# Optimization experiments

Measured on AMD Instinct MI355X. Metric: run time of the kernel, lower is better.

## Reference

```python
import jax, jax.numpy as jnp
import numpy as np

N = 50000      # nodes per graph
E = 800000     # edges per graph (avg degree 16)
IN = 128       # in_dim
OUT = 64       # out_dim
HEADS = 2      # second GCNConv out = OUT*HEADS = 128
FILL = 2.0     # improved=True self-loop weight


def setup_inputs():
    key = jax.random.key(0)
    ks = jax.random.split(key, 10)
    x1 = jax.random.normal(ks[0], (N, IN), jnp.float32)
    edge_index1 = jax.random.randint(ks[1], (2, E), 0, N)
    edge_weight1 = jax.random.uniform(ks[2], (E,), jnp.float32)
    x2 = jax.random.normal(ks[3], (N, IN), jnp.float32)
    edge_index2 = jax.random.randint(ks[4], (2, E), 0, N)
    edge_weight2 = jax.random.uniform(ks[5], (E,), jnp.float32)
    # shared tower params (source bug: gcn1 used for both inputs)
    W1 = jax.random.normal(ks[6], (IN, OUT), jnp.float32) / np.sqrt(IN)
    b1 = jnp.zeros((OUT,), jnp.float32)
    W2 = jax.random.normal(ks[7], (OUT, OUT * HEADS), jnp.float32) / np.sqrt(OUT)
    b2 = jnp.zeros((OUT * HEADS,), jnp.float32)
    return {"x1": x1, "edge_index1": edge_index1, "edge_weight1": edge_weight1,
            "x2": x2, "edge_index2": edge_index2, "edge_weight2": edge_weight2,
            "W1": W1, "b1": b1, "W2": W2, "b2": b2}


def _gcn_conv(x, src, dst, ew, W, b, n):
    # GCNConv(improved=True, add_self_loops=True, aggr='max')
    loop = jnp.arange(n)
    src = jnp.concatenate([src, loop])
    dst = jnp.concatenate([dst, loop])
    ew = jnp.concatenate([ew, jnp.full((n,), FILL, ew.dtype)])
    # symmetric gcn normalization
    deg = jax.ops.segment_sum(ew, dst, num_segments=n)
    dinv = jnp.where(deg > 0, jax.lax.rsqrt(jnp.maximum(deg, 1e-30)), 0.0)
    norm = dinv[src] * ew * dinv[dst]          # [E+N]
    h = x @ W                                   # [N, F_out]
    msg = norm[:, None] * h[src]                # [E+N, F_out] gathered messages
    out = jax.ops.segment_max(msg, dst, num_segments=n)  # scatter-max
    out = jnp.where(jnp.isfinite(out), out, 0.0)          # guard empty segments
    return out + b


def _tower(x, ei, ew, W1, b1, W2, b2):
    ew = jax.nn.relu(ew)
    h = _gcn_conv(x, ei[0], ei[1], ew, W1, b1, x.shape[0])
    return _gcn_conv(h, ei[0], ei[1], ew, W2, b2, x.shape[0])


def reference(x1, edge_index1, edge_weight1, x2, edge_index2, edge_weight2, W1, b1, W2, b2):
    g1 = _tower(x1, edge_index1, edge_weight1, W1, b1, W2, b2)
    g2 = _tower(x2, edge_index2, edge_weight2, W1, b1, W2, b2)
    return (g1, g2)
```

## Files before the change

### kernel.cpp

```cpp
#include <hip/hip_runtime.h>
#include <hip/hip_fp16.h>

static constexpr float FILLW = 2.0f;
static constexpr int BSH  = 6;
static constexpr int CAPB = 1792;
static constexpr int NPB  = 256;
static constexpr int EPT  = 8;

__device__ __forceinline__ unsigned pk_mul(unsigned a, unsigned b){
    unsigned r; asm("v_pk_mul_f16 %0, %1, %2" : "=v"(r) : "v"(a), "v"(b)); return r;
}
__device__ __forceinline__ unsigned pk_max(unsigned a, unsigned b){
    unsigned r; asm("v_pk_max_f16 %0, %1, %2" : "=v"(r) : "v"(a), "v"(b)); return r;
}

template<int F, int K, int TR, int KC, bool SCALE, typename OutT>
__device__ __forceinline__ void gemm_tile(const float* __restrict__ A,
        const float* __restrict__ W, OutT* __restrict__ C,
        const float* __restrict__ dv, int rb, int N,
        float* __restrict__ Ws, float* __restrict__ As){
    constexpr int NCH = K / KC;
    constexpr int TRp = TR + 4;
    constexpr int CG  = F / 8;
    constexpr int LPT = TR * KC / 1024;
    const int tid = threadIdx.x;
    for (int i = tid; i < K * F / 4; i += 256)
        ((float4*)Ws)[i] = ((const float4*)W)[i];
    const int tx = tid % CG, ty = tid / CG;
    const int c0 = tx * 8, r0 = ty * 8;

    float acc[8][8];
    #pragma unroll
    for (int i = 0; i < 8; ++i)
        #pragma unroll
        for (int j = 0; j < 8; ++j) acc[i][j] = 0.f;

    float4 st[LPT];
    auto gload = [&](int kc){
        #pragma unroll
        for (int l2 = 0; l2 < LPT; ++l2){
            int l = l2 * 256 + tid;
            int r = l / (KC / 4);
            int kk = (l % (KC / 4)) * 4;
            int ar = rb + r; if (ar >= N) ar = N - 1;
            st[l2] = *(const float4*)(A + (size_t)ar * K + kc * KC + kk);
        }
    };
    auto swrite = [&](int buf){
        float* p = As + buf * (KC * TRp);
        #pragma unroll
        for (int l2 = 0; l2 < LPT; ++l2){
            int l = l2 * 256 + tid;
            int r = l / (KC / 4);
            int kk = (l % (KC / 4)) * 4;
            p[(kk+0)*TRp + r] = st[l2].x;
            p[(kk+1)*TRp + r] = st[l2].y;
            p[(kk+2)*TRp + r] = st[l2].z;
            p[(kk+3)*TRp + r] = st[l2].w;
        }
    };

    gload(0); swrite(0);
    __syncthreads();
    for (int kc = 0; kc < NCH; ++kc){
        if (kc + 1 < NCH) gload(kc + 1);
        const float* Ab = As + (kc & 1) * (KC * TRp);
        #pragma unroll
        for (int j = 0; j < KC; ++j){
            const float* wrow = Ws + (kc * KC + j) * F + c0;
            float4 w0 = *(const float4*)(wrow);
            float4 w1 = *(const float4*)(wrow + 4);
            float4 a0 = *(const float4*)(Ab + j * TRp + r0);
            float4 a1 = *(const float4*)(Ab + j * TRp + r0 + 4);
            float av[8] = {a0.x,a0.y,a0.z,a0.w,a1.x,a1.y,a1.z,a1.w};
            float wvv[8] = {w0.x,w0.y,w0.z,w0.w,w1.x,w1.y,w1.z,w1.w};
            #pragma unroll
            for (int rr = 0; rr < 8; ++rr)
                #pragma unroll
                for (int cc = 0; cc < 8; ++cc)
                    acc[rr][cc] = fmaf(av[rr], wvv[cc], acc[rr][cc]);
        }
        if (kc + 1 < NCH){ swrite((kc + 1) & 1); __syncthreads(); }
    }
    #pragma unroll
    for (int rr = 0; rr < 8; ++rr){
        int row = rb + r0 + rr;
        if (row < N){
            float scv = 1.0f;
            if constexpr (SCALE) scv = dv[row];
            if constexpr (sizeof(OutT) == 2){
                __half2 o2[4];
                #pragma unroll
                for (int q = 0; q < 4; ++q)
                    o2[q] = __floats2half2_rn(acc[rr][2*q]*scv, acc[rr][2*q+1]*scv);
                *(float4*)((__half*)C + (size_t)row * F + c0) = *(float4*)o2;
            } else {
                float4 o0 = {acc[rr][0]*scv, acc[rr][1]*scv, acc[rr][2]*scv, acc[rr][3]*scv};
                float4 o1 = {acc[rr][4]*scv, acc[rr][5]*scv, acc[rr][6]*scv, acc[rr][7]*scv};
                *(float4*)((float*)C + (size_t)row * F + c0)     = o0;
                *(float4*)((float*)C + (size_t)row * F + c0 + 4) = o1;
            }
        }
    }
}

__device__ __forceinline__ void xcd_map(int c, int TW2, int LIN_BPT,
                                        int& t, int& chunk){
    if (TW2){ int x = c & 7; t = x >> 2; chunk = (c >> 3) * 4 + (x & 3); }
    else    { t = c / LIN_BPT; chunk = c - t * LIN_BPT; }
}

__global__ void __launch_bounds__(256) k_cg1(const float* __restrict__ x0,
        const float* __restrict__ x1, const float* __restrict__ W1,
        __half* __restrict__ h0, __half* __restrict__ h1,
        const int* __restrict__ dst0, const int* __restrict__ dst1,
        int* __restrict__ cnts,
        int N, int E, int BPT, int GB, int B1, int TW2){
    __shared__ float Ws[64 * 128];
    __shared__ float As[2 * 8 * 260];
    if ((int)blockIdx.x < GB){
        int t  = (int)blockIdx.x / BPT;
        int rb = ((int)blockIdx.x - t * BPT) * 256;
        gemm_tile<64,128,256,8,false,__half>(t ? x1 : x0, W1, t ? h1 : h0,
                                             nullptr, rb, N, Ws, As);
        return;
    }
    int t, blk;
    xcd_map((int)blockIdx.x - GB, TW2, NPB, t, blk);
    const int* dst = t ? dst1 : dst0;
    int* hist = (int*)Ws;
    const int tid = threadIdx.x;
    for (int i = tid; i < B1; i += 256) hist[i] = 0;
    __syncthreads();
    int per = (E + NPB - 1) / NPB;
    int e0 = blk * per;
    int e1 = e0 + per; if (e1 > E) e1 = E;
    for (int e = e0 + tid; e < e1; e += 256 * EPT){
        int dl[EPT];
        #pragma unroll
        for (int q = 0; q < EPT; ++q){ int ee = e + q*256; dl[q] = (ee < e1) ? dst[ee] : -1; }
        #pragma unroll
        for (int q = 0; q < EPT; ++q) if (dl[q] >= 0) atomicAdd(&hist[dl[q] >> BSH], 1);
    }
    __syncthreads();
    int* co = cnts + (size_t)(t * NPB + blk) * B1;
    for (int i = tid; i < B1; i += 256) co[i] = hist[i];
}

__global__ void __launch_bounds__(64) k_scanR(int* __restrict__ cnts,
        int* __restrict__ gcnt, int B1){
    int bid = (int)blockIdx.x;
    int t = bid / B1, b = bid % B1;
    int lane = threadIdx.x;
    int* cp = cnts + (size_t)t * NPB * B1 + b;
    int x[4];
    #pragma unroll
    for (int j = 0; j < 4; ++j) x[j] = cp[(size_t)(lane * 4 + j) * B1];
    int s = x[0] + x[1] + x[2] + x[3];
    int sc = s;
    #pragma unroll
    for (int o = 1; o < 64; o <<= 1){ int u = __shfl_up(sc, o); if (lane >= o) sc += u; }
    int e0 = sc - s;
    int e1 = e0 + x[0], e2 = e1 + x[1], e3 = e2 + x[2];
    cp[(size_t)(lane * 4 + 0) * B1] = e0;
    cp[(size_t)(lane * 4 + 1) * B1] = e1;
    cp[(size_t)(lane * 4 + 2) * B1] = e2;
    cp[(size_t)(lane * 4 + 3) * B1] = e3;
    if (lane == 63) gcnt[t * B1 + b] = sc;
}

__global__ void __launch_bounds__(256) k_scatter(const int* __restrict__ src0,
        const int* __restrict__ src1,
        const int* __restrict__ dst0, const int* __restrict__ dst1,
        const float* __restrict__ ew0, const float* __restrict__ ew1,
        const int* __restrict__ cnts, uint2* __restrict__ stage,
        int N, int E, int B1, int TW2){
    __shared__ int hist[1024];
    int t, blk;
    xcd_map((int)blockIdx.x, TW2, NPB, t, blk);
    const int* src = t ? src1 : src0;
    const int* dst = t ? dst1 : dst0;
    const float* ew = t ? ew1 : ew0;
    uint2* stg = stage + (size_t)t * B1 * CAPB;
    const int* co = cnts + (size_t)(t * NPB + blk) * B1;
    const int tid = threadIdx.x;
    for (int i = tid; i < B1; i += 256) hist[i] = co[i];
    __syncthreads();
    int per = (E + NPB - 1) / NPB;
    int e0 = blk * per;
    int e1 = e0 + per; if (e1 > E) e1 = E;
    for (int e = e0 + tid; e < e1; e += 256 * EPT){
        int dl[EPT], sl[EPT]; float wl[EPT];
        #pragma unroll
        for (int q = 0; q < EPT; ++q){
            int ee = e + q*256;
            if (ee < e1){ dl[q] = dst[ee]; sl[q] = src[ee]; wl[q] = fmaxf(ew[ee], 0.f); }
            else dl[q] = -1;
        }
        int r[EPT];
        #pragma unroll
        for (int q = 0; q < EPT; ++q)
            if (dl[q] >= 0) r[q] = atomicAdd(&hist[dl[q] >> BSH], 1);
        #pragma unroll
        for (int q = 0; q < EPT; ++q)
            if (dl[q] >= 0 && r[q] < CAPB)
                stg[(size_t)(dl[q] >> BSH) * CAPB + r[q]] =
                    make_uint2(__float_as_uint(wl[q]),
                               (unsigned)sl[q] | ((unsigned)(dl[q] & 63) << 16));
    }
}

__global__ void __launch_bounds__(256) k_pack(const uint2* __restrict__ stage,
        const int* __restrict__ gcnt, int* __restrict__ woff,
        uint2* __restrict__ sn, float* __restrict__ dinv,
        __half* __restrict__ h1, int N, int E, int B1, int TW2){
    int t, b;
    xcd_map((int)blockIdx.x, TW2, B1, t, b);
    if (b >= B1) return;
    const int tid = threadIdx.x;
    const uint2* stg = stage + (size_t)t * B1 * CAPB;
    const int* gc = gcnt + t * B1;
    __shared__ int   wsum[4];
    __shared__ int   nh[64];
    __shared__ float nw[64];
    __shared__ int   offs[64];
    __shared__ float dvs[64];
    int acc = 0;
    for (int i = tid; i < b; i += 256) acc += gc[i];
    #pragma unroll
    for (int o = 32; o; o >>= 1) acc += __shfl_down(acc, o);
    int lane = tid & 63, wv = tid >> 6;
    if (lane == 0) wsum[wv] = acc;
    if (tid < 64){ nh[tid] = 0; nw[tid] = 0.f; }
    __syncthreads();
    const int base = wsum[0] + wsum[1] + wsum[2] + wsum[3];
    int cnt = gc[b]; if (cnt > CAPB) cnt = CAPB;

    int   rr[7]; uint2 rec[7];
    #pragma unroll
    for (int q = 0; q < 7; ++q){
        int j = q * 256 + tid;
        if (j < cnt){
            uint2 v = stg[(size_t)b * CAPB + j];
            int nl = (v.y >> 16) & 63;
            rr[q] = atomicAdd(&nh[nl], 1);
            atomicAdd(&nw[nl], __uint_as_float(v.x));
            rec[q] = v;
        } else rec[q].y = 0xFFFFFFFFu;
    }
    __syncthreads();
    if (tid < 64){
        int v = nh[tid], sc = v;
        #pragma unroll
        for (int o = 1; o < 64; o <<= 1){ int u = __shfl_up(sc, o); if (tid >= o) sc += u; }
        offs[tid] = sc - v;
        int n = (b << BSH) + tid;
        float dv = 0.f;
        if (n < N){
            dv = rsqrtf(FILLW + nw[tid]);
            woff[t * N + n] = base + sc - v;
            dinv[t * N + n] = dv;
        }
        dvs[tid] = dv;
    }
    __syncthreads();
    uint2* sno = sn + (size_t)t * E;
    #pragma unroll
    for (int q = 0; q < 7; ++q){
        if (rec[q].y != 0xFFFFFFFFu){
            int nl   = (int)((rec[q].y >> 16) & 63);
            unsigned srcv = rec[q].y & 0xFFFFu;
            __half hw = __float2half(__uint_as_float(rec[q].x));
            unsigned hu = (unsigned)__half_as_ushort(hw);
            sno[(size_t)base + offs[nl] + rr[q]] =
                make_uint2(srcv, hu | (hu << 16));
        }
    }
    __half2* hb = (__half2*)(h1 + ((size_t)t * N + ((size_t)b << BSH)) * 64);
    #pragma unroll
    for (int j = 0; j < 8; ++j){
        int idx = j * 256 + tid;
        int r = idx >> 5, cc = idx & 31;
        if ((b << BSH) + r < N){
            float2 f = __half22float2(hb[r * 32 + cc]);
            float dv = dvs[r];
            hb[r * 32 + cc] = __floats2half2_rn(f.x * dv, f.y * dv);
        }
    }
}

__global__ void __launch_bounds__(256) k_gemm2(const float* __restrict__ A0,
        const float* __restrict__ A1, const float* __restrict__ W,
        __half* __restrict__ C0, __half* __restrict__ C1,
        const float* __restrict__ dinv, int N, int BPT){
    __shared__ float Ws[64 * 128];
    __shared__ float As[2 * 16 * 132];
    int t  = (int)blockIdx.x / BPT;
    int rb = ((int)blockIdx.x - t * BPT) * 128;
    gemm_tile<128,64,128,16,true,__half>(t ? A1 : A0, W, t ? C1 : C0,
                                         dinv + t * N, rb, N, Ws, As);
}

template<int F, int UG>
__global__ void __launch_bounds__(256) k_agg(const int* __restrict__ woff,
        const uint2* __restrict__ sn, const float* __restrict__ dinv,
        const __half* __restrict__ H0, const __half* __restrict__ H1,
        const float* __restrict__ bias, float* __restrict__ O0, float* __restrict__ O1,
        int N, int E, int BPT, int TW2){
    constexpr int LPR = F / 8;
    constexpr int EG  = 64 / LPR;
    const int lane = threadIdx.x & 63, wv = threadIdx.x >> 6;
    int t, chunk;
    xcd_map((int)blockIdx.x, TW2, BPT, t, chunk);
    int n = chunk * 4 + wv;
    if (n >= N) return;
    int g = t * N + n;
    int beg = woff[g];
    int end = (n == N - 1) ? E : woff[g + 1];
    float di = dinv[g];
    int cnt = end - beg;
    const uint2* st = sn + (size_t)t * E;
    const __half* H = t ? H1 : H0;
    float* O = t ? O1 : O0;
    const int fl = lane % LPR;
    const int eg = lane / LPR;

    unsigned acc[4];
    {
        float4 hv = *(const float4*)(H + (size_t)n * F + fl * 8);
        const unsigned* hp = (const unsigned*)&hv;
        const unsigned two2 = 0x40004000u;
        #pragma unroll
        for (int k = 0; k < 4; ++k) acc[k] = pk_mul(hp[k], two2);
    }
    for (int base = 0; base < cnt; base += 64){
        int m = cnt - base; if (m > 64) m = 64;
        uint2 er = make_uint2(0u, 0u);
        if (lane < m) er = st[beg + base + lane];
        int es = (int)er.x;
        int ep = (int)er.y;
        for (int j = 0; j < m; j += EG * UG){
            int sl[UG], wl[UG]; float4 hv[UG];
            #pragma unroll
            for (int u = 0; u < UG; ++u){
                int jj = j + u * EG + eg; if (jj > m - 1) jj = m - 1;
                sl[u] = __shfl(es, jj);
                wl[u] = __shfl(ep, jj);
            }
            #pragma unroll
            for (int u = 0; u < UG; ++u)
                hv[u] = *(const float4*)(H + (size_t)sl[u] * F + fl * 8);
            #pragma unroll
            for (int u = 0; u < UG; ++u){
                const unsigned* hp = (const unsigned*)&hv[u];
                unsigned w2 = (unsigned)wl[u];
                #pragma unroll
                for (int k = 0; k < 4; ++k)
                    acc[k] = pk_max(acc[k], pk_mul(hp[k], w2));
            }
        }
    }
    #pragma unroll
    for (int msk = LPR; msk < 64; msk <<= 1)
        #pragma unroll
        for (int k = 0; k < 4; ++k){
            unsigned o = (unsigned)__shfl_xor((int)acc[k], msk);
            acc[k] = pk_max(acc[k], o);
        }
    if constexpr (F == 128){
        int f0 = fl * 8 + eg * 2;
        float2 f = __half22float2(*(__half2*)&acc[eg]);
        float2 bb = *(const float2*)(bias + f0);
        *(float2*)(O + (size_t)n * F + f0) =
            make_float2(di * f.x + bb.x, di * f.y + bb.y);
    } else {
        int f0 = fl * 8 + eg;
        unsigned av = acc[eg >> 1];
        unsigned short hs = (unsigned short)((eg & 1) ? (av >> 16) : (av & 0xFFFFu));
        float v = __half2float(__ushort_as_half(hs));
        O[(size_t)n * F + f0] = di * v + bias[f0];
    }
}


extern "C" void kernel_launch(void* const* d_in, const int* in_sizes, int n_in,
                              void* d_out, int out_size, void* d_ws, size_t ws_size,
                              hipStream_t stream){
    const int E  = in_sizes[2];
    const int F1 = in_sizes[7];
    const int F2 = in_sizes[9];
    const int IN = in_sizes[6] / F1;
    const int N  = in_sizes[0] / IN;
    const int B1 = (N + 63) >> BSH;

    const float* W1 = (const float*)d_in[6];
    const float* b1 = (const float*)d_in[7];
    const float* W2 = (const float*)d_in[8];
    const float* b2 = (const float*)d_in[9];

    auto need = [&](int G){
        return (size_t)G * E * 8
             + (size_t)G * N * F2 * 2
             + (size_t)G * N * F1 * 4
             + (size_t)G * N * 8
             + (size_t)G * B1 * 4
             + (size_t)G * NPB * B1 * 4
             + 4096;
    };
    const int G = (ws_size >= need(2)) ? 2 : 1;
    const int TW2 = (G == 2);

    uint2*  sn    = (uint2*)d_ws;
    __half* hbuf  = (__half*)(sn + (size_t)G * E);
    float*  out1  = (float*)(hbuf + (size_t)G * N * F2);
    uint2*  stage = (uint2*)out1;
    float*  dinv  = out1 + (size_t)G * N * F1;
    int*    woff  = (int*)(dinv + (size_t)G * N);
    int*    gcnt  = woff + (size_t)G * N;
    int*    cnts  = gcnt + (size_t)G * B1;

    const int BPT1 = (N + 255) / 256;
    const int BPT2 = (N + 127) / 128;
    const int ABT  = (N + 3) / 4;
    const int GB   = G * BPT1;
    const int partGrid = TW2 ? (NPB / 4) * 8          : G * NPB;
    const int packGrid = TW2 ? ((B1 + 3) / 4) * 8     : G * B1;
    const int aggGrid  = TW2 ? ((ABT + 3) / 4) * 8    : G * ABT;

    for (int it = 0; it < 2; it += G){
        int t0 = it, t1 = (G == 2) ? it + 1 : it;
        const float* x0 = (const float*)d_in[t0*3], * x1 = (const float*)d_in[t1*3];
        const int* ei0 = (const int*)d_in[t0*3+1], * ei1 = (const int*)d_in[t1*3+1];
        const float* ew0 = (const float*)d_in[t0*3+2], * ew1 = (const float*)d_in[t1*3+2];
        const int* src0 = ei0, * dst0 = ei0 + E;
        const int* src1 = ei1, * dst1 = ei1 + E;
        __half* h1_0 = hbuf, * h1_1 = hbuf + (size_t)(G-1) * N * F1;
        __half* h2_0 = hbuf, * h2_1 = hbuf + (size_t)(G-1) * N * F2;
        float* o1_0 = out1, * o1_1 = out1 + (size_t)(G-1) * N * F1;
        float* go0 = (float*)d_out + (size_t)t0 * N * F2;
        float* go1 = (float*)d_out + (size_t)t1 * N * F2;

        k_cg1<<<GB + partGrid, 256, 0, stream>>>(x0, x1, W1, h1_0, h1_1,
                                                 dst0, dst1, cnts, N, E, BPT1, GB, B1, TW2);
        k_scanR<<<G * B1, 64, 0, stream>>>(cnts, gcnt, B1);
        k_scatter<<<partGrid, 256, 0, stream>>>(src0, src1, dst0, dst1, ew0, ew1,
                                                cnts, stage, N, E, B1, TW2);
        k_pack<<<packGrid, 256, 0, stream>>>(stage, gcnt, woff, sn, dinv, hbuf,
                                             N, E, B1, TW2);
        k_agg<64,8><<<aggGrid, 256, 0, stream>>>(woff, sn, dinv, h1_0, h1_1, b1,
                                                 o1_0, o1_1, N, E, ABT, TW2);
        k_gemm2<<<G * BPT2, 256, 0, stream>>>(o1_0, o1_1, W2, h2_0, h2_1, dinv, N, BPT2);
        k_agg<128,4><<<aggGrid, 256, 0, stream>>>(woff, sn, dinv, h2_0, h2_1, b2,
                                                  go0, go1, N, E, ABT, TW2);
    }
}
```

Measured before the change: 349.0 us.

## Sub-bin edges by source range and add range-ordered second aggregation kernel

```diff
diff --git a/kernel.cpp b/kernel.cpp
--- a/kernel.cpp
+++ b/kernel.cpp
@@ -14,13 +14,13 @@
     unsigned r; asm("v_pk_max_f16 %0, %1, %2" : "=v"(r) : "v"(a), "v"(b)); return r;
 }
 
-template<int F, int K, int TR, int KC, bool SCALE, typename OutT>
+template<int F, int K, int TR, int KC, int PAD, bool SCALE, typename OutT>
 __device__ __forceinline__ void gemm_tile(const float* __restrict__ A,
         const float* __restrict__ W, OutT* __restrict__ C,
         const float* __restrict__ dv, int rb, int N,
         float* __restrict__ Ws, float* __restrict__ As){
     constexpr int NCH = K / KC;
-    constexpr int TRp = TR + 4;
+    constexpr int TRp = TR + PAD;
     constexpr int CG  = F / 8;
     constexpr int LPT = TR * KC / 1024;
     const int tid = threadIdx.x;
@@ -117,12 +117,12 @@
         int* __restrict__ cnts,
         int N, int E, int BPT, int GB, int B1, int TW2){
     __shared__ float Ws[64 * 128];
-    __shared__ float As[2 * 8 * 260];
+    __shared__ float As[2 * 8 * 256];
     if ((int)blockIdx.x < GB){
         int t  = (int)blockIdx.x / BPT;
         int rb = ((int)blockIdx.x - t * BPT) * 256;
-        gemm_tile<64,128,256,8,false,__half>(t ? x1 : x0, W1, t ? h1 : h0,
-                                             nullptr, rb, N, Ws, As);
+        gemm_tile<64,128,256,8,0,false,__half>(t ? x1 : x0, W1, t ? h1 : h0,
+                                               nullptr, rb, N, Ws, As);
         return;
     }
     int t, blk;
@@ -212,8 +212,8 @@
 
 __global__ void __launch_bounds__(256) k_pack(const uint2* __restrict__ stage,
         const int* __restrict__ gcnt, int* __restrict__ woff,
-        uint2* __restrict__ sn, float* __restrict__ dinv,
-        __half* __restrict__ h1, int N, int E, int B1, int TW2){
+        int* __restrict__ roff, uint2* __restrict__ sn, float* __restrict__ dinv,
+        __half* __restrict__ h1, int N, int E, int B1, int NPAD, int TW2){
     int t, b;
     xcd_map((int)blockIdx.x, TW2, B1, t, b);
     if (b >= B1) return;
@@ -221,9 +221,9 @@
     const uint2* stg = stage + (size_t)t * B1 * CAPB;
     const int* gc = gcnt + t * B1;
     __shared__ int   wsum[4];
-    __shared__ int   nh[64];
+    __shared__ int   ssum[4];
+    __shared__ int   nh[512];
     __shared__ float nw[64];
-    __shared__ int   offs[64];
     __shared__ float dvs[64];
     int acc = 0;
     for (int i = tid; i < b; i += 256) acc += gc[i];
@@ -231,7 +231,8 @@
     for (int o = 32; o; o >>= 1) acc += __shfl_down(acc, o);
     int lane = tid & 63, wv = tid >> 6;
     if (lane == 0) wsum[wv] = acc;
-    if (tid < 64){ nh[tid] = 0; nw[tid] = 0.f; }
+    nh[tid] = 0; nh[tid + 256] = 0;
+    if (tid < 64) nw[tid] = 0.f;
     __syncthreads();
     const int base = wsum[0] + wsum[1] + wsum[2] + wsum[3];
     int cnt = gc[b]; if (cnt > CAPB) cnt = CAPB;
@@ -242,26 +243,41 @@
         int j = q * 256 + tid;
         if (j < cnt){
             uint2 v = stg[(size_t)b * CAPB + j];
-            int nl = (v.y >> 16) & 63;
-            rr[q] = atomicAdd(&nh[nl], 1);
+            int nl  = (v.y >> 16) & 63;
+            int bin = nl * 8 + (int)((v.y & 0xFFFFu) >> 13);
+            rr[q] = atomicAdd(&nh[bin], 1);
             atomicAdd(&nw[nl], __uint_as_float(v.x));
             rec[q] = v;
         } else rec[q].y = 0xFFFFFFFFu;
     }
     __syncthreads();
+    int c0n = nh[2*tid], c1n = nh[2*tid+1];
+    int s2 = c0n + c1n, sc2 = s2;
+    #pragma unroll
+    for (int o = 1; o < 64; o <<= 1){ int u = __shfl_up(sc2, o); if (lane >= o) sc2 += u; }
+    if (lane == 63) ssum[wv] = sc2;
+    __syncthreads();
+    int wb2 = 0;
+    #pragma unroll
+    for (int k = 0; k < 4; ++k) if (k < wv) wb2 += ssum[k];
+    int excl = wb2 + sc2 - s2;
+    nh[2*tid]   = excl;
+    nh[2*tid+1] = excl + c0n;
+    __syncthreads();
     if (tid < 64){
-        int v = nh[tid], sc = v;
-        #pragma unroll
-        for (int o = 1; o < 64; o <<= 1){ int u = __shfl_up(sc, o); if (tid >= o) sc += u; }
-        offs[tid] = sc - v;
         int n = (b << BSH) + tid;
         float dv = 0.f;
         if (n < N){
             dv = rsqrtf(FILLW + nw[tid]);
-            woff[t * N + n] = base + sc - v;
+            woff[t * N + n] = base + nh[tid * 8];
             dinv[t * N + n] = dv;
         }
         dvs[tid] = dv;
+    }
+    {
+        int* ro = roff + ((size_t)t * NPAD + ((size_t)b << BSH)) * 8;
+        ro[tid]       = base + nh[tid];
+        ro[tid + 256] = base + nh[tid + 256];
     }
     __syncthreads();
     uint2* sno = sn + (size_t)t * E;
@@ -270,9 +286,10 @@
         if (rec[q].y != 0xFFFFFFFFu){
             int nl   = (int)((rec[q].y >> 16) & 63);
             unsigned srcv = rec[q].y & 0xFFFFu;
+            int bin  = nl * 8 + (int)(srcv >> 13);
             __half hw = __float2half(__uint_as_float(rec[q].x));
             unsigned hu = (unsigned)__half_as_ushort(hw);
-            sno[(size_t)base + offs[nl] + rr[q]] =
+            sno[(size_t)base + nh[bin] + rr[q]] =
                 make_uint2(srcv, hu | (hu << 16));
         }
     }
@@ -289,16 +306,16 @@
     }
 }
 
-__global__ void __launch_bounds__(256) k_gemm2(const float* __restrict__ A0,
+__global__ void __launch_bounds__(256, 4) k_gemm2(const float* __restrict__ A0,
         const float* __restrict__ A1, const float* __restrict__ W,
         __half* __restrict__ C0, __half* __restrict__ C1,
         const float* __restrict__ dinv, int N, int BPT){
     __shared__ float Ws[64 * 128];
-    __shared__ float As[2 * 16 * 132];
+    __shared__ float As[2 * 8 * 128];
     int t  = (int)blockIdx.x / BPT;
     int rb = ((int)blockIdx.x - t * BPT) * 128;
-    gemm_tile<128,64,128,16,true,__half>(t ? A1 : A0, W, t ? C1 : C0,
-                                         dinv + t * N, rb, N, Ws, As);
+    gemm_tile<128,64,128,8,0,true,__half>(t ? A1 : A0, W, t ? C1 : C0,
+                                          dinv + t * N, rb, N, Ws, As);
 }
 
 template<int F, int UG>
@@ -382,6 +399,92 @@
     }
 }
 
+template<int UG>
+__global__ void __launch_bounds__(256) k_agg2(const int* __restrict__ roff,
+        const uint2* __restrict__ sn, const float* __restrict__ dinv,
+        const __half* __restrict__ H0, const __half* __restrict__ H1,
+        const float* __restrict__ bias, float* __restrict__ O0, float* __restrict__ O1,
+        int N, int E, int BPT, int NPAD, int TW2){
+    const int lane = threadIdx.x & 63, wv = threadIdx.x >> 6;
+    int t, chunk;
+    xcd_map((int)blockIdx.x, TW2, BPT, t, chunk);
+    int n0 = chunk * 32 + wv * 8;
+    if (n0 >= N) return;
+    const uint2* st = sn + (size_t)t * E;
+    const __half* H = t ? H1 : H0;
+    float* O = t ? O1 : O0;
+    const int fl = lane & 15, eg = lane >> 4;
+    const int* ro = roff + ((size_t)t * NPAD + n0) * 8;
+    int off_l = ro[lane];
+    int off_e = ro[64];
+
+    unsigned acc[8][4];
+    #pragma unroll
+    for (int k = 0; k < 8; ++k){
+        int n = n0 + k; if (n > N - 1) n = N - 1;
+        float4 hv = *(const float4*)(H + (size_t)n * 128 + fl * 8);
+        const unsigned* hp = (const unsigned*)&hv;
+        #pragma unroll
+        for (int i = 0; i < 4; ++i) acc[k][i] = pk_mul(hp[i], 0x40004000u);
+    }
+    for (int rng = 0; rng < 8; ++rng){
+        #pragma unroll
+        for (int k = 0; k < 8; ++k){
+            int bi = k * 8 + rng;
+            int beg = __shfl(off_l, bi);
+            int end = (bi == 63) ? off_e : __shfl(off_l, bi + 1);
+            for (int base = beg; base < end; base += 64){
+                int m = end - base; if (m > 64) m = 64;
+                uint2 er = make_uint2(0u, 0u);
+                if (lane < m) er = st[base + lane];
+                int es = (int)er.x;
+                int ep = (int)er.y;
+                for (int j = 0; j < m; j += 4 * UG){
+                    int sl[UG], wl[UG]; float4 hv[UG];
+                    #pragma unroll
+                    for (int u = 0; u < UG; ++u){
+                        int jj = j + u * 4 + eg; if (jj > m - 1) jj = m - 1;
+                        sl[u] = __shfl(es, jj);
+                        wl[u] = __shfl(ep, jj);
+                    }
+                    #pragma unroll
+                    for (int u = 0; u < UG; ++u)
+                        hv[u] = *(const float4*)(H + (size_t)sl[u] * 128 + fl * 8);
+                    #pragma unroll
+                    for (int u = 0; u < UG; ++u){
+                        const unsigned* hp = (const unsigned*)&hv[u];
+                        unsigned w2 = (unsigned)wl[u];
+                        #pragma unroll
+                        for (int i = 0; i < 4; ++i)
+                            acc[k][i] = pk_max(acc[k][i], pk_mul(hp[i], w2));
+                    }
+                }
+            }
+        }
+    }
+    #pragma unroll
+    for (int k = 0; k < 8; ++k){
+        #pragma unroll
+        for (int msk = 16; msk < 64; msk <<= 1)
+            #pragma unroll
+            for (int i = 0; i < 4; ++i){
+                unsigned o = (unsigned)__shfl_xor((int)acc[k][i], msk);
+                acc[k][i] = pk_max(acc[k][i], o);
+            }
+        int n = n0 + k;
+        if (n < N){
+            float di = dinv[t * N + n];
+            unsigned av = (eg == 0) ? acc[k][0] : (eg == 1) ? acc[k][1]
+                        : (eg == 2) ? acc[k][2] : acc[k][3];
+            int f0 = fl * 8 + eg * 2;
+            float2 f = __half22float2(*(__half2*)&av);
+            float2 bb = *(const float2*)(bias + f0);
+            *(float2*)(O + (size_t)n * 128 + f0) =
+                make_float2(di * f.x + bb.x, di * f.y + bb.y);
+        }
+    }
+}
+
 
 extern "C" void kernel_launch(void* const* d_in, const int* in_sizes, int n_in,
                               void* d_out, int out_size, void* d_ws, size_t ws_size,
@@ -392,6 +495,7 @@
     const int IN = in_sizes[6] / F1;
     const int N  = in_sizes[0] / IN;
     const int B1 = (N + 63) >> BSH;
+    const int NPAD = B1 << BSH;
 
     const float* W1 = (const float*)d_in[6];
     const float* b1 = (const float*)d_in[7];
@@ -405,6 +509,7 @@
              + (size_t)G * N * 8
              + (size_t)G * B1 * 4
              + (size_t)G * NPB * B1 * 4
+             + (size_t)G * NPAD * 8 * 4
              + 4096;
     };
     const int G = (ws_size >= need(2)) ? 2 : 1;
@@ -418,14 +523,17 @@
     int*    woff  = (int*)(dinv + (size_t)G * N);
     int*    gcnt  = woff + (size_t)G * N;
     int*    cnts  = gcnt + (size_t)G * B1;
+    int*    roffg = cnts + (size_t)G * NPB * B1;
 
     const int BPT1 = (N + 255) / 256;
     const int BPT2 = (N + 127) / 128;
     const int ABT  = (N + 3) / 4;
+    const int ABT2 = (N + 31) / 32;
     const int GB   = G * BPT1;
     const int partGrid = TW2 ? (NPB / 4) * 8          : G * NPB;
     const int packGrid = TW2 ? ((B1 + 3) / 4) * 8     : G * B1;
     const int aggGrid  = TW2 ? ((ABT + 3) / 4) * 8    : G * ABT;
+    const int agg2Grid = TW2 ? ((ABT2 + 3) / 4) * 8   : G * ABT2;
 
     for (int it = 0; it < 2; it += G){
         int t0 = it, t1 = (G == 2) ? it + 1 : it;
@@ -445,12 +553,12 @@
         k_scanR<<<G * B1, 64, 0, stream>>>(cnts, gcnt, B1);
         k_scatter<<<partGrid, 256, 0, stream>>>(src0, src1, dst0, dst1, ew0, ew1,
                                                 cnts, stage, N, E, B1, TW2);
-        k_pack<<<packGrid, 256, 0, stream>>>(stage, gcnt, woff, sn, dinv, hbuf,
-                                             N, E, B1, TW2);
-        k_agg<64,8><<<aggGrid, 256, 0, stream>>>(woff, sn, dinv, h1_0, h1_1, b1,
+        k_pack<<<packGrid, 256, 0, stream>>>(stage, gcnt, woff, roffg, sn, dinv, hbuf,
+                                             N, E, B1, NPAD, TW2);
+        k_agg<64,4><<<aggGrid, 256, 0, stream>>>(woff, sn, dinv, h1_0, h1_1, b1,
                                                  o1_0, o1_1, N, E, ABT, TW2);
         k_gemm2<<<G * BPT2, 256, 0, stream>>>(o1_0, o1_1, W2, h2_0, h2_1, dinv, N, BPT2);
-        k_agg<128,4><<<aggGrid, 256, 0, stream>>>(woff, sn, dinv, h2_0, h2_1, b2,
-                                                  go0, go1, N, E, ABT, TW2);
-    }
-}
+        k_agg2<2><<<agg2Grid, 256, 0, stream>>>(roffg, sn, dinv, h2_0, h2_1, b2,
+                                                go0, go1, N, E, ABT2, NPAD, TW2);
+    }
+}
```

After: 482.9 us. 38.3% more time.
